# Kernel tuning notes

Hardware: AMD Instinct MI355X
Metric: run time of the kernel (lower is better)

The kernel has to match this reference:

```python
import math
import jax, jax.numpy as jnp
import numpy as np

MAX_ELL = 3
SLICES = [slice(0, 1), slice(1, 4), slice(4, 9), slice(9, 16)]
LM = 16  # sum(2l+1) for l=0..3
AVG_NEIGH = 16.0


def _f(n):
    return math.factorial(int(n))


def _su2_cg(j1, j2, j3, m1, m2, m3):
    if m3 != m1 + m2:
        return 0.0
    vmin = int(max(-j1 + j2 + m3, -j1 + m1, 0))
    vmax = int(min(j2 + j3 + m1, j3 - j1 + j2, j3 + m3))
    C = (math.sqrt((2 * j3 + 1) * _f(j3 + j1 - j2) * _f(j3 - j1 + j2) * _f(j1 + j2 - j3) / _f(j1 + j2 + j3 + 1))
         * math.sqrt(_f(j3 + m3) * _f(j3 - m3) / (_f(j1 - m1) * _f(j1 + m1) * _f(j2 - m2) * _f(j2 + m2))))
    S = 0.0
    for v in range(vmin, vmax + 1):
        S += ((-1) ** (v + j2 + m2) * _f(j2 + j3 + m1 - v) * _f(j1 - m1 + v)
              / (_f(v) * _f(j3 - j1 + j2 - v) * _f(j3 + m3 - v) * _f(v + j1 - j2 - m3)))
    return C * S


def _qmat(l):
    # real -> complex spherical harmonic change of basis (e3nn convention)
    q = np.zeros((2 * l + 1, 2 * l + 1), dtype=np.complex128)
    for m in range(-l, 0):
        q[l + m, l + abs(m)] = 1.0 / math.sqrt(2)
        q[l + m, l - abs(m)] = -1j / math.sqrt(2)
    q[l, l] = 1.0
    for m in range(1, l + 1):
        q[l + m, l + abs(m)] = (-1) ** m / math.sqrt(2)
        q[l + m, l - abs(m)] = 1j * (-1) ** m / math.sqrt(2)
    return ((-1j) ** l) * q


def _real_cg(l1, l2, l3):
    Cc = np.zeros((2 * l1 + 1, 2 * l2 + 1, 2 * l3 + 1), dtype=np.complex128)
    for i, m1 in enumerate(range(-l1, l1 + 1)):
        for j, m2 in enumerate(range(-l2, l2 + 1)):
            for k, m3 in enumerate(range(-l3, l3 + 1)):
                Cc[i, j, k] = _su2_cg(l1, l2, l3, m1, m2, m3)
    C = np.einsum('ij,kl,mn,ikm->jln', _qmat(l1), _qmat(l2), np.conj(_qmat(l3)), Cc)
    return np.real(C).astype(np.float32)


# all parity-allowed CG paths for o3_restricted interaction irreps (l1+l2+l3 even)
PATHS = []
for _l1 in range(MAX_ELL + 1):
    for _l2 in range(MAX_ELL + 1):
        for _l3 in range(abs(_l1 - _l2), min(MAX_ELL, _l1 + _l2) + 1):
            if (_l1 + _l2 + _l3) % 2 == 0:
                PATHS.append((_l1, _l2, _l3, jnp.asarray(_real_cg(_l1, _l2, _l3))))
NPATH = len(PATHS)  # 23


def _sph(v):
    # component-normalized real spherical harmonics up to l=3, [E,16]
    r = jnp.linalg.norm(v, axis=-1, keepdims=True) + 1e-9
    u = v / r
    x, y, z = u[:, 0], u[:, 1], u[:, 2]
    s3, s5, s15 = math.sqrt(3.0), math.sqrt(5.0), math.sqrt(15.0)
    cols = [jnp.ones_like(x),
            s3 * y, s3 * z, s3 * x,
            s15 * x * y, s15 * y * z, (s5 / 2) * (3 * z * z - 1), s15 * x * z, (s15 / 2) * (x * x - y * y),
            math.sqrt(35.0 / 8.0) * y * (3 * x * x - y * y), math.sqrt(105.0) * x * y * z,
            math.sqrt(21.0 / 8.0) * y * (5 * z * z - 1), (math.sqrt(7.0) / 2) * z * (5 * z * z - 3),
            math.sqrt(21.0 / 8.0) * x * (5 * z * z - 1), (math.sqrt(105.0) / 2) * z * (x * x - y * y),
            math.sqrt(35.0 / 8.0) * x * (x * x - 3 * y * y)]
    return jnp.stack(cols, axis=-1)


def _radial(r, num=8, p=6):
    # Bessel radial basis (cutoff=1.0) with polynomial envelope of degree p
    n = jnp.arange(1, num + 1, dtype=r.dtype)
    rb = math.sqrt(2.0) * jnp.sin(jnp.pi * n * r[:, None]) / (r[:, None] + 1e-9)
    a, b, c = -(p + 1) * (p + 2) / 2.0, float(p * (p + 2)), -p * (p + 1) / 2.0
    env = (1.0 + a * r ** p + b * r ** (p + 1) + c * r ** (p + 2)) * (r < 1.0)
    return rb * env[:, None]


def _lin(W, h):
    # per-l linear mixing of channels: W [4,F,F], h [N,F,16]
    return jnp.concatenate([jnp.einsum('fg,ngm->nfm', W[l], h[:, :, SLICES[l]]) for l in range(4)], axis=-1)


def _lin_sp(Wsp, h, sp):
    # per-species per-l linear: Wsp [S,4,F,F]
    W = Wsp[sp]  # [N,4,F,F]
    return jnp.concatenate([jnp.einsum('nfg,ngm->nfm', W[:, l], h[:, :, SLICES[l]]) for l in range(4)], axis=-1)


def _forward(vectors, node_species, senders, receivers, embed_W, skip_W, lin1_W,
             radial_W1, radial_W2, lin2_W, skip_first_W, prodW1, prodW2, prodW3,
             prod_lin_W, ro_W, mlp_W1, mlp_W2):
    N = node_species.shape[0]
    E = vectors.shape[0]
    F = embed_W.shape[1]
    eps = 1.0 / jnp.sqrt(1.0 + AVG_NEIGH)  # varepsilon init = sqrt(avg_num_neighbors)
    r = jnp.linalg.norm(vectors, axis=-1)
    Ysh = _sph(vectors)          # [E,16]
    rbf = _radial(r)             # [E,8]
    # per-species scalar node embedding into 0e channel
    h = jnp.zeros((N, F, LM), vectors.dtype).at[:, :, 0].set(embed_W[node_species])
    total = jnp.zeros((N,), vectors.dtype)
    L = lin1_W.shape[0]
    for i in range(L):
        first, last = i == 0, i == L - 1
        sc = _lin_sp(skip_W[i], h, node_species) if not first else None
        # interaction: linear -> CG tensor product with Y(r_hat) weighted by radial MLP -> scatter
        h1 = _lin(lin1_W[i], h)
        Rw = (jax.nn.silu(rbf @ radial_W1[i]) @ radial_W2[i]).reshape(E, NPATH, F)
        hs = h1[senders]  # [E,F,16]
        msg = jnp.zeros((E, F, LM), vectors.dtype)
        for p, (l1, l2, l3, C) in enumerate(PATHS):
            msg = msg.at[:, :, SLICES[l3]].add(
                jnp.einsum('ijk,efi,ej,ef->efk', C, hs[:, :, SLICES[l1]], Ysh[:, SLICES[l2]], Rw[:, p, :]))
        h = jax.ops.segment_sum(msg, receivers, num_segments=N)
        h = _lin(lin2_W[i], h) * eps
        if first:
            h = _lin_sp(skip_first_W, h, node_species)
        # symmetric tensor product basis up to correlation 3, per-species weights
        A = h
        w2 = prodW2[i][node_species]  # [N,P,F]
        w3 = prodW3[i][node_species]
        B2 = jnp.zeros_like(A)
        for p, (l1, l2, l3, C) in enumerate(PATHS):
            B2 = B2.at[:, :, SLICES[l3]].add(
                jnp.einsum('ijk,nfi,nfj,nf->nfk', C, A[:, :, SLICES[l1]], A[:, :, SLICES[l2]], w2[:, p, :]))
        B3 = jnp.zeros_like(A)
        for p, (l1, l2, l3, C) in enumerate(PATHS):
            B3 = B3.at[:, :, SLICES[l3]].add(
                jnp.einsum('ijk,nfi,nfj,nf->nfk', C, B2[:, :, SLICES[l1]], A[:, :, SLICES[l2]], w3[:, p, :]))
        h = A * prodW1[i][node_species][:, :, None] + B2 + B3
        h = _lin(prod_lin_W[i], h)
        if sc is not None:
            h = h + sc
        if not last:
            total = total + h[:, :, 0] @ ro_W                    # linear readout
        else:
            total = total + (jax.nn.silu(h[:, :, 0] @ mlp_W1) @ mlp_W2)[:, 0]  # nonlinear readout
    return total


def setup_inputs() -> dict:
    N, E, F, S, H, L = 4096, 65536, 64, 10, 64, 2
    key = jax.random.key(0)
    ks = jax.random.split(key, 20)
    inp = {
        'vectors': 0.25 * jax.random.normal(ks[0], (E, 3), jnp.float32),
        'senders': jax.random.randint(ks[1], (E,), 0, N),
        'receivers': jax.random.randint(ks[2], (E,), 0, N),
        'node_species': jax.random.randint(ks[3], (N,), 0, S),
        'embed_W': jax.random.normal(ks[4], (S, F), jnp.float32),
        'skip_W': jax.random.normal(ks[5], (L, S, 4, F, F), jnp.float32) / math.sqrt(F),
        'lin1_W': jax.random.normal(ks[6], (L, 4, F, F), jnp.float32) / math.sqrt(F),
        'radial_W1': jax.random.normal(ks[7], (L, 8, H), jnp.float32) / math.sqrt(8.0),
        'radial_W2': jax.random.normal(ks[8], (L, H, NPATH * F), jnp.float32) / math.sqrt(H),
        'lin2_W': jax.random.normal(ks[9], (L, 4, F, F), jnp.float32) / math.sqrt(F),
        'skip_first_W': jax.random.normal(ks[10], (S, 4, F, F), jnp.float32) / math.sqrt(F),
        'prodW1': jax.random.normal(ks[11], (L, S, F), jnp.float32),
        'prodW2': 0.1 * jax.random.normal(ks[12], (L, S, NPATH, F), jnp.float32),
        'prodW3': 0.05 * jax.random.normal(ks[13], (L, S, NPATH, F), jnp.float32),
        'prod_lin_W': jax.random.normal(ks[14], (L, 4, F, F), jnp.float32) / math.sqrt(F),
        'ro_W': jax.random.normal(ks[15], (F,), jnp.float32) / math.sqrt(F),
        'mlp_W1': jax.random.normal(ks[16], (F, 16), jnp.float32) / math.sqrt(F),
        'mlp_W2': jax.random.normal(ks[17], (16, 1), jnp.float32) / 4.0,
    }
    return inp


def reference(vectors, senders, receivers, node_species, embed_W, skip_W, lin1_W,
              radial_W1, radial_W2, lin2_W, skip_first_W, prodW1, prodW2, prodW3,
              prod_lin_W, ro_W, mlp_W1, mlp_W2):
    return _forward(vectors, node_species, senders, receivers, embed_W, skip_W, lin1_W,
                    radial_W1, radial_W2, lin2_W, skip_first_W, prodW1, prodW2, prodW3,
                    prod_lin_W, ro_W, mlp_W1, mlp_W2)
```

## Files before the change

### kernel.cpp

```cpp
#include <hip/hip_runtime.h>
#include <cstdint>
#include <cstring>
#include <cmath>

#define NEDGE 65536
#define NNODE 4096
#define FDIM  64
#define LMDIM 16
#define NPATHS 23
#define HDIM  64
#define NSPEC 10
#define RWN   (NPATHS*FDIM)
#define NF16  ((size_t)NNODE * FDIM * LMDIM)
#define STGCAP 17088
#define CHUNKN 1024
#define NCHUNK (NNODE/CHUNKN)
#define NWAVE 4
#define LINB  8

typedef __attribute__((ext_vector_type(8))) short bf16x8;
typedef __attribute__((ext_vector_type(4))) float f32x4;

__device__ __forceinline__ unsigned short f32_to_bf16_rne(float v)
{
    uint32_t bits;
    __builtin_memcpy(&bits, &v, 4);
    bits += 0x7fffu + ((bits >> 16) & 1u);
    return (unsigned short)(bits >> 16);
}


struct cxd { double re, im; };
constexpr cxd cmul_(cxd a, cxd b){ return {a.re*b.re - a.im*b.im, a.re*b.im + a.im*b.re}; }
constexpr cxd cadd_(cxd a, cxd b){ return {a.re + b.re, a.im + b.im}; }

constexpr double csqrt_(double x)
{
    if (x <= 0.0) return 0.0;
    double g = (x < 1.0) ? 1.0 : x;
    for (int i = 0; i < 30; i++) g = 0.5*(g + x/g);
    return g;
}

constexpr double su2_c_(int j1, int j2, int j3, int m1, int m2, int m3,
                        const double* F)
{
    if (m1 + m2 != m3) return 0.0;
    int vmin = -j1 + j2 + m3; if (-j1 + m1 > vmin) vmin = -j1 + m1; if (vmin < 0) vmin = 0;
    int vmax = j2 + j3 + m1; if (j3 - j1 + j2 < vmax) vmax = j3 - j1 + j2; if (j3 + m3 < vmax) vmax = j3 + m3;
    double C = csqrt_((2.0*j3 + 1.0) * F[j3+j1-j2] * F[j3-j1+j2] * F[j1+j2-j3] / F[j1+j2+j3+1])
             * csqrt_(F[j3+m3] * F[j3-m3] / (F[j1-m1] * F[j1+m1] * F[j2-m2] * F[j2+m2]));
    double S = 0.0;
    for (int v = vmin; v <= vmax; v++) {
        double t = F[j2+j3+m1-v] * F[j1-m1+v]
                 / (F[v] * F[j3-j1+j2-v] * F[j3+m3-v] * F[v+j1-j2-m3]);
        S += (((v + j2 + m2) & 1) ? -1.0 : 1.0) * t;
    }
    return C * S;
}

struct QM { cxd q[7][7]; };

constexpr QM qmat_c_(int l)
{
    QM Q{};
    double is2 = 1.0 / csqrt_(2.0);
    for (int m = -l; m < 0; m++) {
        Q.q[l+m][l-m] = cxd{is2, 0.0};
        Q.q[l+m][l+m] = cxd{0.0, -is2};
    }
    Q.q[l][l] = cxd{1.0, 0.0};
    for (int m = 1; m <= l; m++) {
        double s = (m & 1) ? -1.0 : 1.0;
        Q.q[l+m][l+m] = cxd{s*is2, 0.0};
        Q.q[l+m][l-m] = cxd{0.0, s*is2};
    }
    cxd ph = (l==0) ? cxd{1,0} : (l==1) ? cxd{0,-1} : (l==2) ? cxd{-1,0} : cxd{0,1};
    for (int a = 0; a < 7; a++)
        for (int b = 0; b < 7; b++)
            Q.q[a][b] = cmul_(Q.q[a][b], ph);
    return Q;
}

template<int L1, int L2, int L3>
struct CGPath { float v[(2*L1+1)*(2*L2+1)*(2*L3+1)]; };

template<int L1, int L2, int L3>
constexpr CGPath<L1,L2,L3> make_path_()
{
    constexpr int d1 = 2*L1+1, d2 = 2*L2+1, d3 = 2*L3+1;
    CGPath<L1,L2,L3> R{};
    double F[16] = {};
    F[0] = 1.0;
    for (int i = 1; i < 16; i++) F[i] = F[i-1] * i;
    QM q1 = qmat_c_(L1), q2 = qmat_c_(L2), q3 = qmat_c_(L3);
    double Cc[7][7][7] = {};
    for (int i = 0; i < d1; i++)
    for (int k = 0; k < d2; k++)
    for (int m = 0; m < d3; m++)
        Cc[i][k][m] = su2_c_(L1, L2, L3, i-L1, k-L2, m-L3, F);
    for (int jj = 0; jj < d1; jj++)
    for (int bb = 0; bb < d2; bb++)
    for (int cc = 0; cc < d3; cc++) {
        cxd s{0.0, 0.0};
        for (int i = 0; i < d1; i++) {
            cxd a = q1.q[i][jj];
            if (a.re == 0.0 && a.im == 0.0) continue;
            for (int k = 0; k < d2; k++) {
                cxd b = q2.q[k][bb];
                if (b.re == 0.0 && b.im == 0.0) continue;
                for (int m = 0; m < d3; m++) {
                    cxd g = q3.q[m][cc];
                    if (g.re == 0.0 && g.im == 0.0) continue;
                    double cg = Cc[i][k][m];
                    if (cg == 0.0) continue;
                    cxd gc = {g.re*cg, -g.im*cg};
                    s = cadd_(s, cmul_(cmul_(a, b), gc));
                }
            }
        }
        R.v[(jj*d2 + bb)*d3 + cc] = (float)s.re;
    }
    return R;
}

template<int V> struct ic_ { static constexpr int value = V; };
template<int I, int N, typename F>
__device__ __forceinline__ void cfor_(F& f)
{
    if constexpr (I < N) { f(ic_<I>{}); cfor_<I+1, N>(f); }
}
template<int N, typename F>
__device__ __forceinline__ void cfor(F f) { cfor_<0, N>(f); }

template<int L1, int L2, int L3>
__device__ __forceinline__ void spath(const float* __restrict__ a1,
                                      const float* __restrict__ a2,
                                      float w, float* __restrict__ acc)
{
    constexpr CGPath<L1,L2,L3> P = make_path_<L1,L2,L3>();
    constexpr int d2 = 2*L2+1, d3 = 2*L3+1;
    float t[d3];
    #pragma unroll
    for (int k = 0; k < d3; k++) t[k] = 0.f;
    cfor<2*L1+1>([&](auto I) {
        cfor<d2>([&](auto J) {
            constexpr int i = decltype(I)::value;
            constexpr int j = decltype(J)::value;
            float pr = a1[i] * a2[j];
            (void)pr;
            cfor<d3>([&](auto K) {
                constexpr int k = decltype(K)::value;
                constexpr float c = P.v[(i*d2 + j)*d3 + k];
                if constexpr (c > 1e-10f || c < -1e-10f)
                    t[k] = fmaf(c, pr, t[k]);
            });
        });
    });
    #pragma unroll
    for (int k = 0; k < d3; k++) acc[k] = fmaf(w, t[k], acc[k]);
}

#define SALLP(A1, A2, W, ACC)                       \
    spath<0,0,0>(A1+0, A2+0, (W)[ 0], ACC+0);       \
    spath<0,1,1>(A1+0, A2+1, (W)[ 1], ACC+1);       \
    spath<0,2,2>(A1+0, A2+4, (W)[ 2], ACC+4);       \
    spath<0,3,3>(A1+0, A2+9, (W)[ 3], ACC+9);       \
    spath<1,0,1>(A1+1, A2+0, (W)[ 4], ACC+1);       \
    spath<1,1,0>(A1+1, A2+1, (W)[ 5], ACC+0);       \
    spath<1,1,2>(A1+1, A2+1, (W)[ 6], ACC+4);       \
    spath<1,2,1>(A1+1, A2+4, (W)[ 7], ACC+1);       \
    spath<1,2,3>(A1+1, A2+4, (W)[ 8], ACC+9);       \
    spath<1,3,2>(A1+1, A2+9, (W)[ 9], ACC+4);       \
    spath<2,0,2>(A1+4, A2+0, (W)[10], ACC+4);       \
    spath<2,1,1>(A1+4, A2+1, (W)[11], ACC+1);       \
    spath<2,1,3>(A1+4, A2+1, (W)[12], ACC+9);       \
    spath<2,2,0>(A1+4, A2+4, (W)[13], ACC+0);       \
    spath<2,2,2>(A1+4, A2+4, (W)[14], ACC+4);       \
    spath<2,3,1>(A1+4, A2+9, (W)[15], ACC+1);       \
    spath<2,3,3>(A1+4, A2+9, (W)[16], ACC+9);       \
    spath<3,0,3>(A1+9, A2+0, (W)[17], ACC+9);       \
    spath<3,1,2>(A1+9, A2+1, (W)[18], ACC+4);       \
    spath<3,2,1>(A1+9, A2+4, (W)[19], ACC+1);       \
    spath<3,2,3>(A1+9, A2+4, (W)[20], ACC+9);       \
    spath<3,3,0>(A1+9, A2+9, (W)[21], ACC+0);       \
    spath<3,3,2>(A1+9, A2+9, (W)[22], ACC+4);


__global__ void mace_geom_kernel(const float* __restrict__ vec,
                                 float* __restrict__ ysh, float* __restrict__ rbf)
{
    int e = blockIdx.x * blockDim.x + threadIdx.x;
    if (e >= NEDGE) return;
    float x = vec[3*e+0], y = vec[3*e+1], z = vec[3*e+2];
    float r = sqrtf(x*x + y*y + z*z);
    float inv = 1.0f / (r + 1e-9f);
    float ux = x*inv, uy = y*inv, uz = z*inv;

    const float s3    = 1.7320508075688772f;
    const float s5_2  = 1.1180339887498949f;
    const float s15   = 3.8729833462074170f;
    const float s15_2 = 1.9364916731037085f;
    const float s35_8 = 2.0916500663351889f;
    const float s105  = 10.246950765959598f;
    const float s21_8 = 1.6201851746019651f;
    const float s7_2  = 1.3228756555322954f;
    const float s105_2= 5.1234753829797990f;

    float* Y = ysh + (size_t)e * 16;
    Y[0]  = 1.0f;
    Y[1]  = s3 * uy;
    Y[2]  = s3 * uz;
    Y[3]  = s3 * ux;
    Y[4]  = s15 * ux * uy;
    Y[5]  = s15 * uy * uz;
    Y[6]  = s5_2 * (3.f*uz*uz - 1.f);
    Y[7]  = s15 * ux * uz;
    Y[8]  = s15_2 * (ux*ux - uy*uy);
    Y[9]  = s35_8 * uy * (3.f*ux*ux - uy*uy);
    Y[10] = s105 * ux * uy * uz;
    Y[11] = s21_8 * uy * (5.f*uz*uz - 1.f);
    Y[12] = s7_2 * uz * (5.f*uz*uz - 3.f);
    Y[13] = s21_8 * ux * (5.f*uz*uz - 1.f);
    Y[14] = s105_2 * uz * (ux*ux - uy*uy);
    Y[15] = s35_8 * ux * (ux*ux - 3.f*uy*uy);

    float env = 0.f;
    if (r < 1.f) {
        float r2 = r*r, r3 = r2*r, r6 = r3*r3, r7 = r6*r, r8 = r7*r;
        env = 1.f - 28.f*r6 + 48.f*r7 - 21.f*r8;
    }
    const float sq2 = 1.4142135623730951f;
    const float PI_ = 3.14159265358979323846f;
    float* R = rbf + (size_t)e * 8;
    #pragma unroll
    for (int n = 1; n <= 8; n++)
        R[n-1] = sq2 * sinf(PI_ * (float)n * r) * inv * env;
}

__global__ void mace_init_h_kernel(const int* __restrict__ spec,
                                   const float* __restrict__ embed,
                                   float* __restrict__ h)
{
    int idx = blockIdx.x * blockDim.x + threadIdx.x;
    int n = idx >> 10;
    int t = idx & 1023;
    int f = t >> 4, m = t & 15;
    h[idx] = (m == 0) ? embed[spec[n]*FDIM + f] : 0.f;
}

__global__ void mace_radial_kernel(const float* __restrict__ rbf,
                                   const float* __restrict__ W1,
                                   unsigned short* __restrict__ hidb)
{
    int idx = blockIdx.x * blockDim.x + threadIdx.x;
    int e = idx >> 6, j = idx & 63;
    float a = 0.f;
    #pragma unroll
    for (int n = 0; n < 8; n++)
        a = fmaf(rbf[(size_t)e*8 + n], W1[n*64 + j], a);
    hidb[idx] = f32_to_bf16_rne(a / (1.f + expf(-a)));
}

__global__ void w2t_kernel(const float* __restrict__ W2,
                           unsigned short* __restrict__ w2t)
{
    int idx = blockIdx.x * blockDim.x + threadIdx.x;
    if (idx >= RWN*64) return;
    int h = idx & 63, n = idx >> 6;
    w2t[idx] = f32_to_bf16_rne(W2[(size_t)h*RWN + n]);
}


__global__ void csr_hist_kernel(const int* __restrict__ recv, int* __restrict__ cnt)
{
    int e = blockIdx.x * blockDim.x + threadIdx.x;
    if (e < NEDGE) atomicAdd(&cnt[recv[e]], 1);
}

__global__ void csr_scan_kernel(const int* __restrict__ cnt,
                                int* __restrict__ off, int* __restrict__ cur)
{
    __shared__ int part[1024];
    int t = threadIdx.x;
    int v0 = cnt[t*4+0], v1 = cnt[t*4+1], v2 = cnt[t*4+2], v3 = cnt[t*4+3];
    int sum = v0 + v1 + v2 + v3;
    part[t] = sum;
    __syncthreads();
    for (int d = 1; d < 1024; d <<= 1) {
        int x = (t >= d) ? part[t-d] : 0;
        __syncthreads();
        part[t] += x;
        __syncthreads();
    }
    int run = part[t] - sum;
    off[t*4+0] = run; cur[t*4+0] = run; run += v0;
    off[t*4+1] = run; cur[t*4+1] = run; run += v1;
    off[t*4+2] = run; cur[t*4+2] = run; run += v2;
    off[t*4+3] = run; cur[t*4+3] = run; run += v3;
    if (t == 1023) off[4096] = run;
}

__global__ void csr_scatter_kernel(const int* __restrict__ recv,
                                   int* __restrict__ cur, int* __restrict__ eidx)
{
    int e = blockIdx.x * blockDim.x + threadIdx.x;
    if (e < NEDGE) {
        int pos = atomicAdd(&cur[recv[e]], 1);
        eidx[pos] = e;
    }
}


__global__ __launch_bounds__(256) void rw_gemm_chunk(
    const unsigned short* __restrict__ hidb,
    const unsigned short* __restrict__ w2t,
    const int* __restrict__ offs,
    const int* __restrict__ eidx,
    int cb,
    unsigned short* __restrict__ stg)
{
    int coff0 = offs[cb];
    int count = offs[cb + CHUNKN] - coff0;
    if (count > STGCAP) count = STGCAP;
    int e0 = blockIdx.x * 64;
    if (e0 >= count) return;
    int n0 = blockIdx.y * 64;
    int wv = threadIdx.x >> 6;
    int l  = threadIdx.x & 63;
    int lm = l & 15, q = l >> 4;

    const unsigned short* arow = w2t + (size_t)(n0 + wv*16 + lm) * 64 + q*8;
    bf16x8 a0 = *reinterpret_cast<const bf16x8*>(arow);
    bf16x8 a1 = *reinterpret_cast<const bf16x8*>(arow + 32);

    f32x4 acc[4];
    bool val[4];
    int erow[4];
    #pragma unroll
    for (int t = 0; t < 4; t++) {
        int row = e0 + t*16 + lm;
        val[t] = (row < count);
        erow[t] = eidx[coff0 + (val[t] ? row : 0)];
        acc[t] = (f32x4){0.f, 0.f, 0.f, 0.f};
    }
    #pragma unroll
    for (int t = 0; t < 4; t++) {
        const unsigned short* brow = hidb + (size_t)erow[t] * 64 + q*8;
        bf16x8 b0 = *reinterpret_cast<const bf16x8*>(brow);
        bf16x8 b1 = *reinterpret_cast<const bf16x8*>(brow + 32);
        acc[t] = __builtin_amdgcn_mfma_f32_16x16x32_bf16(a0, b0, acc[t], 0, 0, 0);
        acc[t] = __builtin_amdgcn_mfma_f32_16x16x32_bf16(a1, b1, acc[t], 0, 0, 0);
    }

    #pragma unroll
    for (int t = 0; t < 4; t++) {
        if (!val[t]) continue;
        int row = e0 + t*16 + lm;
        unsigned short u[4];
        u[0] = f32_to_bf16_rne(acc[t][0]);
        u[1] = f32_to_bf16_rne(acc[t][1]);
        u[2] = f32_to_bf16_rne(acc[t][2]);
        u[3] = f32_to_bf16_rne(acc[t][3]);
        uint2 pack;
        pack.x = (uint32_t)u[0] | ((uint32_t)u[1] << 16);
        pack.y = (uint32_t)u[2] | ((uint32_t)u[3] << 16);
        *reinterpret_cast<uint2*>(&stg[(size_t)row * RWN + n0 + wv*16 + q*4]) = pack;
    }
}


__global__ __launch_bounds__(512, 2) void mace_lin_kernel(
    const float* __restrict__ in, const float* __restrict__ W,
    const float* __restrict__ add, float* __restrict__ out, float scale)
{
    __shared__ __align__(16) float st[LINB][16*68];
    int nb = blockIdx.x * LINB;
    int tid = threadIdx.x;

    #pragma unroll
    for (int j = 0; j < LINB; j++) {
        size_t base = (size_t)(nb + j) * 1024;
        float2 v = *reinterpret_cast<const float2*>(in + base + tid*2);
        int f = tid >> 3;
        int m = (tid & 7) * 2;
        st[j][m*68 + f]     = v.x;
        st[j][(m+1)*68 + f] = v.y;
    }
    __syncthreads();

    int fp = tid >> 4;
    int m  = tid & 15;
    int l  = (m == 0) ? 0 : (m < 4) ? 1 : (m < 9) ? 2 : 3;
    const float* Wl = W + l*4096;
    int f0 = fp * 2;

    float4 wa[16], wb[16];
    #pragma unroll
    for (int q = 0; q < 16; q++) {
        wa[q] = *reinterpret_cast<const float4*>(Wl + (size_t)f0*64 + q*4);
        wb[q] = *reinterpret_cast<const float4*>(Wl + (size_t)(f0+1)*64 + q*4);
    }

    #pragma unroll
    for (int j = 0; j < LINB; j++) {
        float ax = 0.f, ay = 0.f, az = 0.f, aw = 0.f;
        float bx = 0.f, by = 0.f, bz = 0.f, bw = 0.f;
        #pragma unroll
        for (int q = 0; q < 16; q++) {
            float4 sv = *reinterpret_cast<const float4*>(&st[j][m*68 + q*4]);
            ax = fmaf(wa[q].x, sv.x, ax); ay = fmaf(wa[q].y, sv.y, ay);
            az = fmaf(wa[q].z, sv.z, az); aw = fmaf(wa[q].w, sv.w, aw);
            bx = fmaf(wb[q].x, sv.x, bx); by = fmaf(wb[q].y, sv.y, by);
            bz = fmaf(wb[q].z, sv.z, bz); bw = fmaf(wb[q].w, sv.w, bw);
        }
        float a0 = ((ax + ay) + (az + aw)) * scale;
        float a1 = ((bx + by) + (bz + bw)) * scale;
        size_t o0 = (size_t)(nb + j) * 1024 + (size_t)f0*16 + m;
        if (add) { a0 += add[o0]; a1 += add[o0 + 16]; }
        out[o0] = a0;
        out[o0 + 16] = a1;
    }
}

__device__ __forceinline__ void lin_sp_core(const float* __restrict__ in,
                                            const float* __restrict__ Wbase,
                                            const float* __restrict__ add,
                                            float* __restrict__ out,
                                            int n, int tid)
{
    __shared__ __align__(16) float st[16*68];
    size_t base = (size_t)n * 1024;
    {
        float2 v = *reinterpret_cast<const float2*>(in + base + tid*2);
        int f = tid >> 3;
        int m = (tid & 7) * 2;
        st[m*68 + f]     = v.x;
        st[(m+1)*68 + f] = v.y;
    }
    __syncthreads();
    int fp = tid >> 4;
    int m  = tid & 15;
    int l  = (m == 0) ? 0 : (m < 4) ? 1 : (m < 9) ? 2 : 3;
    const float* Wl = Wbase + l*4096;
    int f0 = fp * 2;
    const float4* wa4 = reinterpret_cast<const float4*>(Wl + (size_t)f0*64);
    const float4* wb4 = reinterpret_cast<const float4*>(Wl + (size_t)(f0+1)*64);
    const float4* sv4 = reinterpret_cast<const float4*>(&st[m*68]);

    float ax = 0.f, ay = 0.f, az = 0.f, aw = 0.f;
    float bx = 0.f, by = 0.f, bz = 0.f, bw = 0.f;
    #pragma unroll
    for (int q = 0; q < 16; q++) {
        float4 sv = sv4[q];
        float4 wa = wa4[q];
        float4 wb = wb4[q];
        ax = fmaf(wa.x, sv.x, ax); ay = fmaf(wa.y, sv.y, ay);
        az = fmaf(wa.z, sv.z, az); aw = fmaf(wa.w, sv.w, aw);
        bx = fmaf(wb.x, sv.x, bx); by = fmaf(wb.y, sv.y, by);
        bz = fmaf(wb.z, sv.z, bz); bw = fmaf(wb.w, sv.w, bw);
    }
    float a0 = (ax + ay) + (az + aw);
    float a1 = (bx + by) + (bz + bw);
    size_t o0 = base + (size_t)f0*16 + m;
    if (add) { a0 += add[o0]; a1 += add[o0 + 16]; }
    out[o0] = a0;
    out[o0 + 16] = a1;
}

__global__ __launch_bounds__(512) void mace_lin_sp_kernel(
    const float* __restrict__ in, const float* __restrict__ Wsp,
    const int* __restrict__ spec, const float* __restrict__ add,
    float* __restrict__ out)
{
    int n = blockIdx.x;
    lin_sp_core(in, Wsp + (size_t)spec[n]*4*4096, add, out, n, threadIdx.x);
}

__global__ __launch_bounds__(256) void compose_kernel(
    const float* __restrict__ skipf, const float* __restrict__ l2W,
    float* __restrict__ Wc, float eps)
{
    int idx = blockIdx.x * 256 + threadIdx.x;
    int g = idx & 63, f = (idx >> 6) & 63, l = (idx >> 12) & 3, sp = idx >> 14;
    const float* A = skipf + ((size_t)sp*4 + l)*4096 + f*64;
    const float* B = l2W + (size_t)l*4096 + g;
    float s0 = 0.f, s1 = 0.f;
    #pragma unroll 8
    for (int k = 0; k < 64; k += 2) {
        s0 = fmaf(A[k],   B[(size_t)k*64],        s0);
        s1 = fmaf(A[k+1], B[(size_t)(k+1)*64],    s1);
    }
    Wc[idx] = (s0 + s1) * eps;
}


__global__ __launch_bounds__(256) void mace_gather_kernel(
    const float* __restrict__ h1,
    const float* __restrict__ ysh,
    const unsigned short* __restrict__ stg,
    const int* __restrict__ senders,
    const int* __restrict__ offs,
    const int* __restrict__ eidx,
    int cb,
    float* __restrict__ out)
{
    int n = cb + blockIdx.x;
    int wv = threadIdx.x >> 6;
    int f  = threadIdx.x & 63;
    __shared__ float red[16][NWAVE*64];

    float acc[16];
    #pragma unroll
    for (int k = 0; k < 16; k++) acc[k] = 0.f;

    int coff0 = offs[cb];
    int ib = offs[n], ie = offs[n+1];

    int idx = ib + wv;
    int e = 0, s = 0;
    if (idx < ie) { e = eidx[idx]; s = senders[e]; }

    for (; idx < ie; idx += NWAVE) {
        int sidx = idx - coff0;
        if (sidx >= STGCAP) break;
        int nidx = idx + NWAVE;
        int en = 0;
        if (nidx < ie) en = eidx[nidx];

        float hv[16];
        {
            const float4* hp4 = reinterpret_cast<const float4*>(
                h1 + (size_t)s*1024 + f*16);
            float4 v0 = hp4[0], v1 = hp4[1], v2 = hp4[2], v3 = hp4[3];
            hv[0]=v0.x; hv[1]=v0.y; hv[2]=v0.z; hv[3]=v0.w;
            hv[4]=v1.x; hv[5]=v1.y; hv[6]=v1.z; hv[7]=v1.w;
            hv[8]=v2.x; hv[9]=v2.y; hv[10]=v2.z; hv[11]=v2.w;
            hv[12]=v3.x; hv[13]=v3.y; hv[14]=v3.z; hv[15]=v3.w;
        }
        float yv[16];
        {
            const float4* yp4 = reinterpret_cast<const float4*>(ysh + (size_t)e*16);
            float4 v0 = yp4[0], v1 = yp4[1], v2 = yp4[2], v3 = yp4[3];
            yv[0]=v0.x; yv[1]=v0.y; yv[2]=v0.z; yv[3]=v0.w;
            yv[4]=v1.x; yv[5]=v1.y; yv[6]=v1.z; yv[7]=v1.w;
            yv[8]=v2.x; yv[9]=v2.y; yv[10]=v2.z; yv[11]=v2.w;
            yv[12]=v3.x; yv[13]=v3.y; yv[14]=v3.z; yv[15]=v3.w;
        }
        float rw[23];
        {
            const unsigned short* rp = stg + (size_t)sidx*RWN + f;
            #pragma unroll
            for (int p = 0; p < NPATHS; p++) {
                uint32_t b = ((uint32_t)rp[p*64]) << 16;
                __builtin_memcpy(&rw[p], &b, 4);
            }
        }
        int sn = 0;
        if (nidx < ie) sn = senders[en];

        SALLP(hv, yv, rw, acc)

        e = en; s = sn;
    }

    #pragma unroll
    for (int k = 0; k < 16; k++) red[k][wv*64 + f] = acc[k];
    __syncthreads();
    if (wv == 0) {
        float* dst = out + (size_t)n*1024 + f*16;
        #pragma unroll
        for (int k = 0; k < 16; k++) {
            float v = 0.f;
            #pragma unroll
            for (int w = 0; w < NWAVE; w++) v += red[k][w*64 + f];
            dst[k] = v;
        }
    }
}


__global__ __launch_bounds__(256) void mace_prod_kernel(
    const float* __restrict__ A,
    const float* __restrict__ w1base,
    const float* __restrict__ w2base,
    const float* __restrict__ w3base,
    const int* __restrict__ spec,
    float* __restrict__ out)
{
    int gid = blockIdx.x * 256 + threadIdx.x;
    int n = gid >> 6, f = gid & 63;

    float a[16];
    {
        const float4* ap = reinterpret_cast<const float4*>(A + (size_t)n*1024 + f*16);
        float4 v0 = ap[0], v1 = ap[1], v2 = ap[2], v3 = ap[3];
        a[0]=v0.x; a[1]=v0.y; a[2]=v0.z; a[3]=v0.w;
        a[4]=v1.x; a[5]=v1.y; a[6]=v1.z; a[7]=v1.w;
        a[8]=v2.x; a[9]=v2.y; a[10]=v2.z; a[11]=v2.w;
        a[12]=v3.x; a[13]=v3.y; a[14]=v3.z; a[15]=v3.w;
    }
    int sp = spec[n];

    float wk[23];
    {
        const float* wp = w2base + (size_t)sp*(NPATHS*64) + f;
        #pragma unroll
        for (int p = 0; p < NPATHS; p++) wk[p] = wp[p*64];
    }
    float b2[16];
    #pragma unroll
    for (int k = 0; k < 16; k++) b2[k] = 0.f;
    SALLP(a, a, wk, b2)

    {
        const float* wp = w3base + (size_t)sp*(NPATHS*64) + f;
        #pragma unroll
        for (int p = 0; p < NPATHS; p++) wk[p] = wp[p*64];
    }
    float b3[16];
    #pragma unroll
    for (int k = 0; k < 16; k++) b3[k] = 0.f;
    SALLP(b2, a, wk, b3)

    float w1 = w1base[sp*64 + f];
    float4* dst4 = reinterpret_cast<float4*>(out + (size_t)n*1024 + f*16);
    float o[16];
    #pragma unroll
    for (int k = 0; k < 16; k++) o[k] = fmaf(a[k], w1, b2[k] + b3[k]);
    dst4[0] = make_float4(o[0], o[1], o[2], o[3]);
    dst4[1] = make_float4(o[4], o[5], o[6], o[7]);
    dst4[2] = make_float4(o[8], o[9], o[10], o[11]);
    dst4[3] = make_float4(o[12], o[13], o[14], o[15]);
}


__global__ void mace_readout0_kernel(const float* __restrict__ h,
                                     const float* __restrict__ roW,
                                     float* __restrict__ out)
{
    int n = blockIdx.x;
    int f = threadIdx.x;
    float v = h[(size_t)n*1024 + f*16] * roW[f];
    #pragma unroll
    for (int o = 32; o > 0; o >>= 1) v += __shfl_down(v, o, 64);
    if (f == 0) out[n] = v;
}

__global__ void mace_readout1_kernel(const float* __restrict__ h,
                                     const float* __restrict__ W1,
                                     const float* __restrict__ W2,
                                     float* __restrict__ out)
{
    int n = blockIdx.x;
    int f = threadIdx.x;
    __shared__ float sx[64];
    __shared__ float sz[16];
    sx[f] = h[(size_t)n*1024 + f*16];
    __syncthreads();
    if (f < 16) {
        float z = 0.f;
        #pragma unroll
        for (int g = 0; g < 64; g++) z = fmaf(sx[g], W1[g*16 + f], z);
        z = z / (1.f + expf(-z));
        sz[f] = z * W2[f];
    }
    __syncthreads();
    if (f == 0) {
        float t = 0.f;
        #pragma unroll
        for (int j = 0; j < 16; j++) t += sz[j];
        out[n] += t;
    }
}


extern "C" void kernel_launch(void* const* d_in, const int* in_sizes, int n_in,
                              void* d_out, int out_size, void* d_ws, size_t ws_size,
                              hipStream_t stream)
{
    const float* vectors = (const float*)d_in[0];
    const int*   senders = (const int*)d_in[1];
    const int*   receivers = (const int*)d_in[2];
    const int*   spec    = (const int*)d_in[3];
    const float* embed_W = (const float*)d_in[4];
    const float* skip_W  = (const float*)d_in[5];
    const float* lin1_W  = (const float*)d_in[6];
    const float* radW1   = (const float*)d_in[7];
    const float* radW2   = (const float*)d_in[8];
    const float* lin2_W  = (const float*)d_in[9];
    const float* skipf_W = (const float*)d_in[10];
    const float* prodW1  = (const float*)d_in[11];
    const float* prodW2  = (const float*)d_in[12];
    const float* prodW3  = (const float*)d_in[13];
    const float* plin_W  = (const float*)d_in[14];
    const float* ro_W    = (const float*)d_in[15];
    const float* mlp_W1  = (const float*)d_in[16];
    const float* mlp_W2  = (const float*)d_in[17];
    float* out = (float*)d_out;

    float* w   = (float*)d_ws;
    float* ysh = w;
    float* rbf = ysh + (size_t)NEDGE * 16;
    float* hid = rbf + (size_t)NEDGE * 8;
    float* t0  = hid + (size_t)NEDGE * 64;
    float* t1  = t0 + NF16;
    float* sc  = t1 + NF16;
    float* h   = sc + NF16;
    float* t2  = h  + NF16;
    float* ext = t2 + NF16;
    unsigned short* hidb = (unsigned short*)hid;
    unsigned short* stg = (unsigned short*)h;
    float* wc  = ext;
    unsigned short* wt = (unsigned short*)(ext + NF16);
    int* cnt  = (int*)((char*)wt + (size_t)RWN*64*2);
    int* offs = cnt + 4096;
    int* cur  = offs + 4097;
    int* eidx = cur + 4096;

    const float EPS = 0.24253562503633297f;

    (void)hipMemsetAsync(cnt, 0, 4096 * sizeof(int), stream);
    csr_hist_kernel<<<NEDGE/256, 256, 0, stream>>>(receivers, cnt);
    csr_scan_kernel<<<1, 1024, 0, stream>>>(cnt, offs, cur);
    csr_scatter_kernel<<<NEDGE/256, 256, 0, stream>>>(receivers, cur, eidx);

    mace_geom_kernel<<<NEDGE/256, 256, 0, stream>>>(vectors, ysh, rbf);
    mace_init_h_kernel<<<(NNODE*1024)/256, 256, 0, stream>>>(spec, embed_W, h);

    dim3 ggrid((STGCAP + 63)/64, NPATHS);

    for (int layer = 0; layer < 2; layer++) {
        const float* W1 = radW1 + (size_t)layer * 8 * HDIM;
        const float* W2 = radW2 + (size_t)layer * HDIM * RWN;
        const float* l1W = lin1_W + (size_t)layer * 4 * FDIM * FDIM;
        const float* l2W = lin2_W + (size_t)layer * 4 * FDIM * FDIM;
        const float* plW = plin_W + (size_t)layer * 4 * FDIM * FDIM;
        const float* pw1 = prodW1 + (size_t)layer * NSPEC * FDIM;
        const float* pw2 = prodW2 + (size_t)layer * NSPEC * NPATHS * FDIM;
        const float* pw3 = prodW3 + (size_t)layer * NSPEC * NPATHS * FDIM;

        if (layer == 1) {
            mace_lin_sp_kernel<<<NNODE, 512, 0, stream>>>(
                h, skip_W + (size_t)1 * NSPEC * 4 * FDIM * FDIM, spec, nullptr, sc);
        }

        mace_radial_kernel<<<(NEDGE*HDIM)/256, 256, 0, stream>>>(rbf, W1, hidb);
        w2t_kernel<<<(RWN*64 + 255)/256, 256, 0, stream>>>(W2, wt);
        mace_lin_kernel<<<NNODE/LINB, 512, 0, stream>>>(h, l1W, nullptr, t0, 1.0f);

        for (int c = 0; c < NCHUNK; c++) {
            int cb = c * CHUNKN;
            rw_gemm_chunk<<<ggrid, 256, 0, stream>>>(hidb, wt, offs, eidx, cb, stg);
            mace_gather_kernel<<<CHUNKN, 256, 0, stream>>>(
                t0, ysh, stg, senders, offs, eidx, cb, t1);
        }

        if (layer == 0) {
            compose_kernel<<<(NSPEC*4*64*64)/256, 256, 0, stream>>>(skipf_W, l2W, wc, EPS);
            mace_lin_sp_kernel<<<NNODE, 512, 0, stream>>>(t1, wc, spec, nullptr, h);
            mace_prod_kernel<<<NNODE/4, 256, 0, stream>>>(h, pw1, pw2, pw3, spec, t1);
            mace_lin_kernel<<<NNODE/LINB, 512, 0, stream>>>(t1, plW, nullptr, h, 1.0f);
            mace_readout0_kernel<<<NNODE, 64, 0, stream>>>(h, ro_W, out);
        } else {
            mace_lin_kernel<<<NNODE/LINB, 512, 0, stream>>>(t1, l2W, nullptr, t2, EPS);
            mace_prod_kernel<<<NNODE/4, 256, 0, stream>>>(t2, pw1, pw2, pw3, spec, t1);
            mace_lin_kernel<<<NNODE/LINB, 512, 0, stream>>>(t1, plW, sc, t0, 1.0f);
            mace_readout1_kernel<<<NNODE, 64, 0, stream>>>(t0, mlp_W1, mlp_W2, out);
        }
    }
}
```

Before: 1.013 ms.

## Sort nodes by species and batch species-linear over 8 nodes per block

Adds a counting-sort of nodes by species (hist, scan, scatter kernels) and rewrites the species-dependent linear kernel to process LINB nodes per block in species-sorted order. Weights are held in registers and reloaded only when the species changes, so weight traffic is amortised over several nodes instead of being reloaded for every node. The cost is three extra small launches, a 64-float4 register footprint that may limit occupancy, and scattered node access.

```diff
diff --git a/kernel.cpp b/kernel.cpp
--- a/kernel.cpp
+++ b/kernel.cpp
@@ -311,6 +311,30 @@
     }
 }
 
+__global__ void sp_hist_kernel(const int* __restrict__ spec, int* __restrict__ scnt)
+{
+    int n = blockIdx.x * blockDim.x + threadIdx.x;
+    if (n < NNODE) atomicAdd(&scnt[spec[n]], 1);
+}
+
+__global__ void sp_scan_kernel(const int* __restrict__ scnt, int* __restrict__ scur)
+{
+    if (threadIdx.x == 0) {
+        int run = 0;
+        for (int s = 0; s < NSPEC; s++) { scur[s] = run; run += scnt[s]; }
+    }
+}
+
+__global__ void sp_scatter_kernel(const int* __restrict__ spec,
+                                  int* __restrict__ scur, int* __restrict__ snode)
+{
+    int n = blockIdx.x * blockDim.x + threadIdx.x;
+    if (n < NNODE) {
+        int pos = atomicAdd(&scur[spec[n]], 1);
+        snode[pos] = n;
+    }
+}
+
 
 __global__ __launch_bounds__(256) void rw_gemm_chunk(
     const unsigned short* __restrict__ hidb,
@@ -423,58 +447,73 @@
     }
 }
 
-__device__ __forceinline__ void lin_sp_core(const float* __restrict__ in,
-                                            const float* __restrict__ Wbase,
-                                            const float* __restrict__ add,
-                                            float* __restrict__ out,
-                                            int n, int tid)
-{
-    __shared__ __align__(16) float st[16*68];
-    size_t base = (size_t)n * 1024;
-    {
+__global__ __launch_bounds__(512, 2) void mace_lin_sp_kernel(
+    const float* __restrict__ in, const float* __restrict__ Wsp,
+    const int* __restrict__ spec, const int* __restrict__ snode,
+    const float* __restrict__ add, float* __restrict__ out)
+{
+    __shared__ __align__(16) float st[LINB][16*68];
+    __shared__ int nodes[LINB];
+    int nb = blockIdx.x * LINB;
+    int tid = threadIdx.x;
+
+    if (tid < LINB) nodes[tid] = snode[nb + tid];
+    __syncthreads();
+
+    #pragma unroll
+    for (int j = 0; j < LINB; j++) {
+        size_t base = (size_t)nodes[j] * 1024;
         float2 v = *reinterpret_cast<const float2*>(in + base + tid*2);
         int f = tid >> 3;
         int m = (tid & 7) * 2;
-        st[m*68 + f]     = v.x;
-        st[(m+1)*68 + f] = v.y;
+        st[j][m*68 + f]     = v.x;
+        st[j][(m+1)*68 + f] = v.y;
     }
     __syncthreads();
+
     int fp = tid >> 4;
     int m  = tid & 15;
     int l  = (m == 0) ? 0 : (m < 4) ? 1 : (m < 9) ? 2 : 3;
-    const float* Wl = Wbase + l*4096;
     int f0 = fp * 2;
-    const float4* wa4 = reinterpret_cast<const float4*>(Wl + (size_t)f0*64);
-    const float4* wb4 = reinterpret_cast<const float4*>(Wl + (size_t)(f0+1)*64);
-    const float4* sv4 = reinterpret_cast<const float4*>(&st[m*68]);
-
-    float ax = 0.f, ay = 0.f, az = 0.f, aw = 0.f;
-    float bx = 0.f, by = 0.f, bz = 0.f, bw = 0.f;
+
+    int sp_cur = spec[nodes[0]];
+    const float* Wl = Wsp + (size_t)sp_cur*4*4096 + l*4096;
+    float4 wa[16], wb[16];
     #pragma unroll
     for (int q = 0; q < 16; q++) {
-        float4 sv = sv4[q];
-        float4 wa = wa4[q];
-        float4 wb = wb4[q];
-        ax = fmaf(wa.x, sv.x, ax); ay = fmaf(wa.y, sv.y, ay);
-        az = fmaf(wa.z, sv.z, az); aw = fmaf(wa.w, sv.w, aw);
-        bx = fmaf(wb.x, sv.x, bx); by = fmaf(wb.y, sv.y, by);
-        bz = fmaf(wb.z, sv.z, bz); bw = fmaf(wb.w, sv.w, bw);
-    }
-    float a0 = (ax + ay) + (az + aw);
-    float a1 = (bx + by) + (bz + bw);
-    size_t o0 = base + (size_t)f0*16 + m;
-    if (add) { a0 += add[o0]; a1 += add[o0 + 16]; }
-    out[o0] = a0;
-    out[o0 + 16] = a1;
-}
-
-__global__ __launch_bounds__(512) void mace_lin_sp_kernel(
-    const float* __restrict__ in, const float* __restrict__ Wsp,
-    const int* __restrict__ spec, const float* __restrict__ add,
-    float* __restrict__ out)
-{
-    int n = blockIdx.x;
-    lin_sp_core(in, Wsp + (size_t)spec[n]*4*4096, add, out, n, threadIdx.x);
+        wa[q] = *reinterpret_cast<const float4*>(Wl + (size_t)f0*64 + q*4);
+        wb[q] = *reinterpret_cast<const float4*>(Wl + (size_t)(f0+1)*64 + q*4);
+    }
+
+    #pragma unroll
+    for (int j = 0; j < LINB; j++) {
+        int spj = spec[nodes[j]];
+        if (spj != sp_cur) {
+            sp_cur = spj;
+            const float* Wl2 = Wsp + (size_t)sp_cur*4*4096 + l*4096;
+            #pragma unroll
+            for (int q = 0; q < 16; q++) {
+                wa[q] = *reinterpret_cast<const float4*>(Wl2 + (size_t)f0*64 + q*4);
+                wb[q] = *reinterpret_cast<const float4*>(Wl2 + (size_t)(f0+1)*64 + q*4);
+            }
+        }
+        float ax = 0.f, ay = 0.f, az = 0.f, aw = 0.f;
+        float bx = 0.f, by = 0.f, bz = 0.f, bw = 0.f;
+        #pragma unroll
+        for (int q = 0; q < 16; q++) {
+            float4 sv = *reinterpret_cast<const float4*>(&st[j][m*68 + q*4]);
+            ax = fmaf(wa[q].x, sv.x, ax); ay = fmaf(wa[q].y, sv.y, ay);
+            az = fmaf(wa[q].z, sv.z, az); aw = fmaf(wa[q].w, sv.w, aw);
+            bx = fmaf(wb[q].x, sv.x, bx); by = fmaf(wb[q].y, sv.y, by);
+            bz = fmaf(wb[q].z, sv.z, bz); bw = fmaf(wb[q].w, sv.w, bw);
+        }
+        float a0 = (ax + ay) + (az + aw);
+        float a1 = (bx + by) + (bz + bw);
+        size_t o0 = (size_t)nodes[j] * 1024 + (size_t)f0*16 + m;
+        if (add) { a0 += add[o0]; a1 += add[o0 + 16]; }
+        out[o0] = a0;
+        out[o0 + 16] = a1;
+    }
 }
 
 __global__ __launch_bounds__(256) void compose_kernel(
@@ -717,6 +756,9 @@
     int* offs = cnt + 4096;
     int* cur  = offs + 4097;
     int* eidx = cur + 4096;
+    int* scnt  = eidx + NEDGE;
+    int* scur  = scnt + 16;
+    int* snode = scur + 16;
 
     const float EPS = 0.24253562503633297f;
 
@@ -724,6 +766,11 @@
     csr_hist_kernel<<<NEDGE/256, 256, 0, stream>>>(receivers, cnt);
     csr_scan_kernel<<<1, 1024, 0, stream>>>(cnt, offs, cur);
     csr_scatter_kernel<<<NEDGE/256, 256, 0, stream>>>(receivers, cur, eidx);
+
+    (void)hipMemsetAsync(scnt, 0, 32 * sizeof(int), stream);
+    sp_hist_kernel<<<NNODE/256, 256, 0, stream>>>(spec, scnt);
+    sp_scan_kernel<<<1, 64, 0, stream>>>(scnt, scur);
+    sp_scatter_kernel<<<NNODE/256, 256, 0, stream>>>(spec, scur, snode);
 
     mace_geom_kernel<<<NEDGE/256, 256, 0, stream>>>(vectors, ysh, rbf);
     mace_init_h_kernel<<<(NNODE*1024)/256, 256, 0, stream>>>(spec, embed_W, h);
@@ -741,8 +788,9 @@
         const float* pw3 = prodW3 + (size_t)layer * NSPEC * NPATHS * FDIM;
 
         if (layer == 1) {
-            mace_lin_sp_kernel<<<NNODE, 512, 0, stream>>>(
-                h, skip_W + (size_t)1 * NSPEC * 4 * FDIM * FDIM, spec, nullptr, sc);
+            mace_lin_sp_kernel<<<NNODE/LINB, 512, 0, stream>>>(
+                h, skip_W + (size_t)1 * NSPEC * 4 * FDIM * FDIM, spec, snode,
+                nullptr, sc);
         }
 
         mace_radial_kernel<<<(NEDGE*HDIM)/256, 256, 0, stream>>>(rbf, W1, hidb);
@@ -758,7 +806,8 @@
 
         if (layer == 0) {
             compose_kernel<<<(NSPEC*4*64*64)/256, 256, 0, stream>>>(skipf_W, l2W, wc, EPS);
-            mace_lin_sp_kernel<<<NNODE, 512, 0, stream>>>(t1, wc, spec, nullptr, h);
+            mace_lin_sp_kernel<<<NNODE/LINB, 512, 0, stream>>>(
+                t1, wc, spec, snode, nullptr, h);
             mace_prod_kernel<<<NNODE/4, 256, 0, stream>>>(h, pw1, pw2, pw3, spec, t1);
             mace_lin_kernel<<<NNODE/LINB, 512, 0, stream>>>(t1, plW, nullptr, h, 1.0f);
             mace_readout0_kernel<<<NNODE, 64, 0, stream>>>(h, ro_W, out);
```

Measured after the change: 992.9 us. No clear change (-1.9%).
